# Optimization experiments

Measured on AMD Instinct MI355X. Metric: run time of the kernel, lower is better.

The kernel has to match this reference:

```python
import jax, jax.numpy as jnp
import numpy as np
from jax import lax

H, W = 2048, 2048
KS = 3            # spatial NMS / centroid kernel size
EPS_NMS = 1e-5    # NMS3d eps (threshold=0 branch)
EPS_DIV = 1e-8
BORDER = 1        # int(mrSize=1.0)


def _grid_weights():
    # generate_3dgrid(3, 3, 3) centered: coords = linspace(-k/2+1, k/2, k) = [-0.5, 0.5, 1.5]
    c = np.linspace(-KS / 2 + 1, KS / 2, KS).astype(np.float32)
    g2 = np.stack([np.repeat(c, KS), np.tile(c, KS)], 1)                              # [9,2] (y,x), y-major
    g3 = np.concatenate([np.repeat(c, KS * KS)[:, None], np.tile(g2, (KS, 1))], 1)    # [27,3] (z,y,x)
    # grid.t().view(3,3,3,3): out-channel c holds coordinate c over the 3x3x3 cube (OIHW)
    return jnp.asarray(g3.T.reshape(3, 3, KS, KS))


def _border_mask():
    m = np.ones((H, W), np.float32)
    m[:BORDER] = 0; m[H - BORDER:] = 0; m[:, :BORDER] = 0; m[:, W - BORDER:] = 0
    return jnp.asarray(m)


def setup_inputs() -> dict:
    key = jax.random.key(0)
    k1, k2, k3, k4 = jax.random.split(key, 4)
    return {
        "low": jax.random.uniform(k1, (1, 1, H, W), jnp.float32),
        "cur": jax.random.uniform(k2, (1, 1, H, W), jnp.float32),
        "high": jax.random.uniform(k3, (1, 1, H, W), jnp.float32),
        "aff_resp": jax.random.normal(k4, (1, 4, H, W), jnp.float32),
        "octaveMap": jnp.zeros((1, 1, H, W), jnp.float32),
        "num_features": 4096,
    }


def _core(low, cur, high, aff_resp, octaveMap, num_features):
    resp3d = jnp.concatenate([low, cur, high], axis=1)  # [1,3,H,W] scale cube
    # MaxPool3d(kernel=3, stride=1, padding=(0,1,1)) over (scale,H,W) -> [1,1,H,W]
    mp = lax.reduce_window(resp3d, -jnp.inf, lax.max,
                           (1, 3, 3, 3), (1, 1, 1, 1),
                           [(0, 0), (0, 0), (1, 1), (1, 1)])
    nms = (resp3d - mp + EPS_NMS > 0).astype(resp3d.dtype) * resp3d  # broadcast over 3 scales
    # keep only the center scale, zero 1px border, mask already-taken octave positions
    nmsed = nms[:, 1:2] * _border_mask() * (1.0 - octaveMap)          # [1,1,H,W]
    vals, idxs = lax.top_k(nmsed.reshape(-1), num_features)          # fixed-k selection branch
    # centroid fit: coordinate-weighted 3x3x3 sums / mass via conv2d over the 3 scale channels
    gw = _grid_weights()
    num = lax.conv_general_dilated(resp3d, gw, (1, 1), [(1, 1), (1, 1)])
    den = lax.conv_general_dilated(resp3d, jnp.ones((3, 3, KS, KS), resp3d.dtype),
                                   (1, 1), [(1, 1), (1, 1)])
    sc = num / (den + EPS_DIV)  # [1,3,H,W] = (scale, dy, dx)
    yy, xx = jnp.meshgrid(jnp.arange(H, dtype=sc.dtype), jnp.arange(W, dtype=sc.dtype), indexing="ij")
    sc = jnp.stack([sc[0, 0], sc[0, 1] + yy, sc[0, 2] + xx], 0).reshape(3, -1).T  # [H*W,3]
    sc = sc[idxs] / jnp.array([float(min(H, W)), float(H), float(W)], sc.dtype)   # normalize (s,y,x)
    A = aff_resp.reshape(4, -1).T[idxs].reshape(-1, 2, 2)   # gather per-keypoint affine
    A = sc[:, 0][:, None, None] * A                          # scale * A
    center_xy = jnp.stack([sc[:, 2], sc[:, 1]], axis=1)[:, :, None]  # (x, y) column
    lafs = jnp.concatenate([A, center_xy], axis=2)           # [K,2,3] LAFs
    return vals, lafs, nmsed


def reference(low, cur, high, aff_resp, octaveMap, num_features):
    vals, lafs, nmsed = _core(low, cur, high, aff_resp, octaveMap, num_features)
    octave_new = (octaveMap + nmsed).astype(jnp.uint8)  # updated octave occupancy map
    return vals, lafs, octave_new
```

## Files before the change

### kernel.cpp

```cpp
#include <hip/hip_runtime.h>
#include <cstdint>
#include <cstddef>

#define HH 2048
#define WW 2048
#define NPIX (HH * WW)
#define EPS_NMS 1e-5f
#define EPS_DIV 1e-8f
#define NEG_INF (-3.402823466e+38f)
#define NMS_THREADS 512
#define ROWS 4
#define LCAP 2048
#define SG_CAP 7936
#define NBIN 2048
#define SEL_BLOCKS 64
#define RB_ELEMS 64
#define BUFCAP 4096
#define T0F 0.99854f

typedef unsigned long long u64;


__device__ __forceinline__ float max3(float a, float b, float c) {
    return fmaxf(a, fmaxf(b, c));
}

__device__ __forceinline__ unsigned int aload(const unsigned int* p) {
    return __hip_atomic_load(p, __ATOMIC_RELAXED, __HIP_MEMORY_SCOPE_AGENT);
}

__device__ __forceinline__ void gbar(char* base) {
    __syncthreads();
    if (threadIdx.x == 0) {
        unsigned int* root = (unsigned int*)base;
        unsigned int* gc = (unsigned int*)(base + 64 + ((blockIdx.x & 7) << 6));
        __threadfence();
        if (atomicAdd(gc, 1u) == 7u) atomicAdd(root, 1u);
        while (aload(root) < 8u) __builtin_amdgcn_s_sleep(1);
        __threadfence();
    }
    __syncthreads();
}

__device__ __forceinline__ void pick_bin(const unsigned int* __restrict__ hg,
                                         unsigned int remk_in,
                                         unsigned int* s,
                                         unsigned int* sh_bin,
                                         unsigned int* sh_rem)
{
    const int tid = threadIdx.x;
    unsigned int bins[8], csum = 0;
    #pragma unroll
    for (int i = 0; i < 8; ++i) { bins[i] = aload(&hg[tid * 8 + i]); csum += bins[i]; }
    s[tid] = csum;
    __syncthreads();
    for (int off = 1; off < 256; off <<= 1) {
        unsigned int v = (tid + off < 256) ? s[tid + off] : 0u;
        __syncthreads(); s[tid] += v; __syncthreads();
    }
    unsigned int incl = s[tid], excl = incl - csum, total = s[0];
    if (tid == 0 && total < remk_in) { *sh_bin = 0u; *sh_rem = remk_in; }
    if (incl >= remk_in && excl < remk_in) {
        unsigned int cum = excl; int b = 7;
        for (; b > 0; --b) { cum += bins[b]; if (cum >= remk_in) break; }
        if (cum < remk_in) cum += bins[0];
        *sh_bin = (unsigned int)(tid * 8 + b);
        *sh_rem = remk_in - (cum - bins[b]);
    }
    __syncthreads();
}

__global__ __launch_bounds__(NMS_THREADS) void nms_map_kernel(
    const float* __restrict__ low, const float* __restrict__ cur,
    const float* __restrict__ high, const float* __restrict__ oct,
    float* __restrict__ oct_out, float* __restrict__ vals_out, int n7k,
    u64* __restrict__ cand, unsigned int* __restrict__ cnt,
    unsigned int* __restrict__ hist0, unsigned int cap)
{
    __shared__ unsigned int lcount, lbase, lT;
    __shared__ unsigned int hl[NBIN];
    __shared__ u64 lcand[LCAP];

    const int tid = threadIdx.x;
    const int lane = tid & 63;
    const int x4 = blockIdx.x * 2048 + tid * 4;
    const int y0 = blockIdx.y * ROWS;
    if (tid == 0) { lcount = 0u; lT = 0u; }
    for (int i = tid; i < NBIN; i += NMS_THREADS) hl[i] = 0u;

    if (blockIdx.y < 16) {
        int n4 = n7k >> 2;
        int i = (int)blockIdx.y * NMS_THREADS + tid;
        float4* vz = (float4*)vals_out;
        if (i < n4) vz[i] = make_float4(0.f, 0.f, 0.f, 0.f);
    }
    __syncthreads();

    float4 Lb[2], Cb[2], Hb[2], Ob[2];
    float eLl[2], eLc[2], eLh[2], eRl[2], eRc[2], eRh[2];

    #define ISSUE(t, slot) {                                                      \
        int tt = (t);                                                             \
        if (tt >= 0 && tt < HH) {                                                 \
            int jj = tt * WW + x4;                                                \
            Lb[slot] = *(const float4*)(low  + jj);                               \
            Cb[slot] = *(const float4*)(cur  + jj);                               \
            Hb[slot] = *(const float4*)(high + jj);                               \
            bool doL = (lane == 0)  && (x4 > 0);                                  \
            bool doR = (lane == 63) && (x4 + 4 < WW);                             \
            eLl[slot] = doL ? low[jj - 1]  : NEG_INF;                             \
            eLc[slot] = doL ? cur[jj - 1]  : NEG_INF;                             \
            eLh[slot] = doL ? high[jj - 1] : NEG_INF;                             \
            eRl[slot] = doR ? low[jj + 4]  : NEG_INF;                             \
            eRc[slot] = doR ? cur[jj + 4]  : NEG_INF;                             \
            eRh[slot] = doR ? high[jj + 4] : NEG_INF;                             \
        } else {                                                                  \
            Lb[slot] = Cb[slot] = Hb[slot] =                                      \
                make_float4(NEG_INF, NEG_INF, NEG_INF, NEG_INF);                  \
            eLl[slot] = eLc[slot] = eLh[slot] = NEG_INF;                          \
            eRl[slot] = eRc[slot] = eRh[slot] = NEG_INF;                          \
        }                                                                         \
    }

    #define CONSUME(slot, hzO, cvO) {                                             \
        float4 l = Lb[slot], c = Cb[slot], hh = Hb[slot];                         \
        float4 z;                                                                 \
        z.x = max3(l.x, c.x, hh.x);                                               \
        z.y = max3(l.y, c.y, hh.y);                                               \
        z.z = max3(l.z, c.z, hh.z);                                               \
        z.w = max3(l.w, c.w, hh.w);                                               \
        float zeL = max3(eLl[slot], eLc[slot], eLh[slot]);                        \
        float zeR = max3(eRl[slot], eRc[slot], eRh[slot]);                        \
        float zl = __shfl_up(z.w, 1, 64);                                         \
        float zr = __shfl_down(z.x, 1, 64);                                       \
        if (lane == 0)  zl = zeL;                                                 \
        if (lane == 63) zr = zeR;                                                 \
        hzO.x = max3(zl,  z.x, z.y);                                              \
        hzO.y = max3(z.x, z.y, z.z);                                              \
        hzO.z = max3(z.y, z.z, z.w);                                              \
        hzO.w = max3(z.z, z.w, zr);                                               \
        cvO = c;                                                                  \
    }

    float4 hzA, hzB, hzC, cvB, cvC, cvT;
    ISSUE(y0 - 1, 0)
    ISSUE(y0,     1)
    Ob[0] = *(const float4*)(oct + y0 * WW + x4);
    CONSUME(0, hzA, cvT)
    ISSUE(y0 + 1, 0)
    CONSUME(1, hzB, cvB)

    #pragma unroll
    for (int j = 0; j < ROWS; ++j) {
        int y = y0 + j;
        if (j + 1 < ROWS) {
            ISSUE(y + 2, (j + 1) & 1)
            Ob[(j + 1) & 1] = *(const float4*)(oct + (y + 1) * WW + x4);
        }
        CONSUME(j & 1, hzC, cvC)

        int idx = y * WW + x4;
        float4 o = Ob[j & 1];
        bool yin = (y > 0) && (y < HH - 1);
        float4 ov;
        #define DO_COMP(comp, i)  {                                               \
            float m = max3(hzA.comp, hzB.comp, hzC.comp);                         \
            int xg = x4 + (i);                                                    \
            bool interior = yin && (xg > 0) && (xg < WW - 1);                     \
            float nm = (((cvB.comp - m + EPS_NMS) > 0.0f) && interior)            \
                       ? cvB.comp * (1.0f - o.comp) : 0.0f;                       \
            ov.comp = (float)((unsigned char)(o.comp + nm));                      \
            if (nm > 0.0f) {                                                      \
                unsigned int p = atomicAdd(&lcount, 1u);                          \
                if (p < LCAP)                                                     \
                    lcand[p] = (((u64)__float_as_uint(nm)) << 32)                 \
                               | (unsigned int)(~(idx + (i)));                    \
            }                                                                     \
        }
        DO_COMP(x, 0) DO_COMP(y, 1) DO_COMP(z, 2) DO_COMP(w, 3)
        #undef DO_COMP
        *(float4*)(oct_out + idx) = ov;
        hzA = hzB; hzB = hzC; cvB = cvC;
    }
    #undef ISSUE
    #undef CONSUME

    __syncthreads();
    unsigned int c = lcount < LCAP ? lcount : LCAP;
    if (tid == 0) lbase = atomicAdd(cnt, c);
    __syncthreads();
    unsigned int base = lbase;
    const u64 T0KEY = ((u64)__float_as_uint(T0F)) << 32;
    unsigned int t0c = 0;
    for (unsigned int i = tid; i < c; i += NMS_THREADS) {
        unsigned int p = base + i;
        if (p < cap) {
            u64 k = lcand[i];
            cand[p] = k;
            atomicAdd(&hl[(unsigned int)(k >> 53)], 1u);
            if (k >= T0KEY) ++t0c;
        }
    }
    if (t0c) atomicAdd(&lT, t0c);
    __syncthreads();
    for (int i = tid; i < NBIN; i += NMS_THREADS) {
        unsigned int v = hl[i];
        if (v) atomicAdd(&hist0[i], v);
    }
    if (tid == 0 && lT) atomicAdd(&cnt[2], lT);
}

__global__ __launch_bounds__(256) void select_rank_kernel(
    const u64* __restrict__ cand, u64* __restrict__ SG,
    unsigned int* __restrict__ cnt,
    const unsigned int* __restrict__ hist0, unsigned int* __restrict__ hist1,
    unsigned int cap, int K,
    const float* __restrict__ low, const float* __restrict__ cur,
    const float* __restrict__ high, const float* __restrict__ aff,
    float* __restrict__ out)
{
    __shared__ u64 sgl[SG_CAP];
    __shared__ unsigned int s[256];
    __shared__ unsigned int rnk[RB_ELEMS];
    __shared__ unsigned int sh_bin, sh_rem, lc, lb;
    unsigned int* h = (unsigned int*)sgl;
    u64* buf = sgl + 2048;

    const int tid = threadIdx.x;
    const int bid = blockIdx.x;
    char* barb = (char*)cnt + 128;
    unsigned int n0 = cnt[0];
    unsigned int n = n0; if (n > cap) n = cap;
    const unsigned int stride = SEL_BLOCKS * 256;
    const u64 T0KEY = ((u64)__float_as_uint(T0F)) << 32;

    unsigned int c2 = cnt[2];
    bool use_fast = (n0 <= cap) && (c2 >= (unsigned int)K) && (c2 <= (unsigned int)SG_CAP);
    unsigned int m = 0;

    if (use_fast) {
        if (tid == 0) lc = 0u;
        __syncthreads();
        for (unsigned int i = bid * 256 + tid; i < n; i += stride) {
            u64 key = cand[i];
            if (key >= T0KEY) {
                unsigned int p = atomicAdd(&lc, 1u);
                if (p < BUFCAP) buf[p] = key;
            }
        }
        __syncthreads();
        unsigned int c = lc;
        if (c > BUFCAP) { if (tid == 0) atomicExch(&cnt[4], 1u); c = BUFCAP; }
        if (tid == 0) lb = atomicAdd(&cnt[5], c);
        __syncthreads();
        unsigned int base = lb;
        for (unsigned int i = tid; i < c; i += 256) {
            unsigned int p = base + i;
            if (p < SG_CAP) SG[p] = buf[i];
        }
        gbar(barb);
        if (aload(&cnt[4]) != 0u) use_fast = false;
        else m = aload(&cnt[5]);
    }

    if (!use_fast) {
        pick_bin(hist0, (unsigned int)K, s, &sh_bin, &sh_rem);
        const unsigned int prefix = sh_bin;
        const unsigned int remk   = sh_rem;

        for (int i = tid; i < NBIN; i += 256) h[i] = 0u;
        __syncthreads();
        for (unsigned int i = bid * 256 + tid; i < n; i += stride) {
            unsigned int k32 = (unsigned int)(cand[i] >> 32);
            if ((k32 >> 21) == prefix) atomicAdd(&h[(k32 >> 10) & (NBIN - 1u)], 1u);
        }
        __syncthreads();
        for (int i = tid; i < NBIN; i += 256) { unsigned int v = h[i]; if (v) atomicAdd(&hist1[i], v); }
        gbar(barb + 576);

        pick_bin(hist1, remk, s, &sh_bin, &sh_rem);
        const unsigned int T = (prefix << 11) | sh_bin;

        if (tid == 0) lc = 0u;
        __syncthreads();
        for (unsigned int i = bid * 256 + tid; i < n; i += stride) {
            u64 key = cand[i];
            if ((unsigned int)(key >> 42) >= T) {
                unsigned int p = atomicAdd(&lc, 1u);
                if (p < BUFCAP) buf[p] = key;
            }
        }
        __syncthreads();
        unsigned int c = lc < BUFCAP ? lc : BUFCAP;
        if (tid == 0) lb = atomicAdd(&cnt[1], c);
        __syncthreads();
        unsigned int base = lb;
        for (unsigned int i = tid; i < c; i += 256) {
            unsigned int p = base + i;
            if (p < SG_CAP) SG[p] = buf[i];
        }
        gbar(barb + 2 * 576);
        m = aload(&cnt[1]); if (m > SG_CAP) m = SG_CAP;
    }

    for (unsigned int i = tid; i < m; i += 256) sgl[i] = SG[i];
    __syncthreads();

    const unsigned int wave = (unsigned int)tid >> 6, lane = (unsigned int)tid & 63u;
    for (unsigned int chunk = (unsigned int)bid * RB_ELEMS; chunk < m;
         chunk += (unsigned int)SEL_BLOCKS * RB_ELEMS) {
        u64 my[16];
        unsigned int r[16];
        #pragma unroll
        for (int i = 0; i < 16; ++i) {
            unsigned int e = chunk + wave * 16 + i;
            my[i] = (e < m) ? sgl[e] : ~0ull;
            r[i] = 0u;
        }
        for (unsigned int j = lane; j < m; j += 64) {
            u64 key = sgl[j];
            #pragma unroll
            for (int i = 0; i < 16; ++i) r[i] += (unsigned int)(key > my[i]);
        }
        #pragma unroll
        for (int i = 0; i < 16; ++i) {
            #pragma unroll
            for (int off = 32; off > 0; off >>= 1)
                r[i] += __shfl_down(r[i], off, 64);
            if (lane == 0) rnk[wave * 16 + i] = r[i];
        }
        __syncthreads();

        if (tid < RB_ELEMS) {
            unsigned int e = chunk + (unsigned int)tid;
            if (e < m) {
                unsigned int rank = rnk[tid];
                if (rank < (unsigned int)K) {
                    u64 my_key = sgl[e];
                    float val = __uint_as_float((unsigned int)(my_key >> 32));
                    unsigned int idx = ~((unsigned int)my_key);
                    out[rank] = val;
                    float* laf = out + K + (size_t)rank * 6;
                    int y = (int)(idx >> 11), x = (int)(idx & (WW - 1));
                    const float ccw[3] = {-0.5f, 0.5f, 1.5f};
                    float den = 0.0f, nz = 0.0f, ny = 0.0f, nx = 0.0f;
                    #pragma unroll
                    for (int dy = -1; dy <= 1; ++dy) {
                        int yy = y + dy;
                        if (yy < 0 || yy >= HH) continue;
                        #pragma unroll
                        for (int dx = -1; dx <= 1; ++dx) {
                            int xx = x + dx;
                            if (xx < 0 || xx >= WW) continue;
                            int jj = yy * WW + xx;
                            float v0 = low[jj], v1 = cur[jj], v2 = high[jj];
                            float ssum = v0 + v1 + v2;
                            den += ssum;
                            nz += -0.5f * v0 + 0.5f * v1 + 1.5f * v2;
                            ny += ccw[dy + 1] * ssum;
                            nx += ccw[dx + 1] * ssum;
                        }
                    }
                    float inv = 1.0f / (den + EPS_DIV);
                    float s_n = (nz * inv) * (1.0f / 2048.0f);
                    float y_n = (ny * inv + (float)y) * (1.0f / 2048.0f);
                    float x_n = (nx * inv + (float)x) * (1.0f / 2048.0f);
                    float a0 = aff[idx], a1 = aff[NPIX + idx];
                    float a2 = aff[2 * NPIX + idx], a3 = aff[3 * NPIX + idx];
                    laf[0] = s_n * a0; laf[1] = s_n * a1; laf[2] = x_n;
                    laf[3] = s_n * a2; laf[4] = s_n * a3; laf[5] = y_n;
                }
            }
        }
        __syncthreads();
    }
}

extern "C" void kernel_launch(void* const* d_in, const int* in_sizes, int n_in,
                              void* d_out, int out_size, void* d_ws, size_t ws_size,
                              hipStream_t stream) {
    const float* low  = (const float*)d_in[0];
    const float* cur  = (const float*)d_in[1];
    const float* high = (const float*)d_in[2];
    const float* aff  = (const float*)d_in[3];
    const float* oct  = (const float*)d_in[4];
    int K = (out_size - NPIX) / 7;
    float* out = (float*)d_out;

    char* ws = (char*)d_ws;
    unsigned int* cnt   = (unsigned int*)ws;
    unsigned int* hist0 = (unsigned int*)(ws + 4096);
    unsigned int* hist1 = (unsigned int*)(ws + 12288);
    u64* SG             = (u64*)(ws + 20480);
    const size_t cand_off = 98304;
    u64* cand           = (u64*)(ws + cand_off);
    size_t cap_sz = ws_size > cand_off ? (ws_size - cand_off) / 8 : 0;
    if (cap_sz > (size_t)NPIX) cap_sz = (size_t)NPIX;
    unsigned int cap = (unsigned int)cap_sz;

    hipMemsetAsync(ws, 0, 20480, stream);

    dim3 gb(WW / 2048, HH / ROWS, 1);
    nms_map_kernel<<<gb, NMS_THREADS, 0, stream>>>(low, cur, high, oct,
                                                   out + (size_t)7 * K,
                                                   out, 7 * K, cand, cnt, hist0, cap);
    select_rank_kernel<<<SEL_BLOCKS, 256, 0, stream>>>(cand, SG, cnt, hist0, hist1,
                                                       cap, K, low, cur, high, aff, out);
}
```

Before: 219.3 us.

## Fuse NMS map and top-k selection into one kernel with last-block crew

Merges the NMS/candidate kernel and the select-rank kernel into one launch. The last 64 blocks to finish the map phase, identified by a ticket counter, become a crew that runs the selection and ranking behind grid barriers. The per-block global histogram build is moved off the hot path into the slow fallback only. Output zeroing now covers only the unfilled ranks, done at the end. The change removes one kernel launch and the histogram atomics, but the crew must spin-wait until all blocks finish, and it relies on all 512 blocks being co-resident or draining in order.

```diff
diff --git a/kernel.cpp b/kernel.cpp
--- a/kernel.cpp
+++ b/kernel.cpp
@@ -8,14 +8,15 @@
 #define EPS_NMS 1e-5f
 #define EPS_DIV 1e-8f
 #define NEG_INF (-3.402823466e+38f)
-#define NMS_THREADS 512
-#define ROWS 4
+#define ROWS 8
 #define LCAP 2048
-#define SG_CAP 7936
+#define SG_CAP 7680
 #define NBIN 2048
-#define SEL_BLOCKS 64
+#define NMS_BLOCKS 512
+#define CREW 64
+#define TICKET_MIN (NMS_BLOCKS - CREW)
 #define RB_ELEMS 64
-#define BUFCAP 4096
+#define BUFCAP 1024
 #define T0F 0.99854f
 
 typedef unsigned long long u64;
@@ -29,11 +30,11 @@
     return __hip_atomic_load(p, __ATOMIC_RELAXED, __HIP_MEMORY_SCOPE_AGENT);
 }
 
-__device__ __forceinline__ void gbar(char* base) {
+__device__ __forceinline__ void gbar(char* base, unsigned int crewid) {
     __syncthreads();
     if (threadIdx.x == 0) {
         unsigned int* root = (unsigned int*)base;
-        unsigned int* gc = (unsigned int*)(base + 64 + ((blockIdx.x & 7) << 6));
+        unsigned int* gc = (unsigned int*)(base + 64 + ((crewid & 7u) << 6));
         __threadfence();
         if (atomicAdd(gc, 1u) == 7u) atomicAdd(root, 1u);
         while (aload(root) < 8u) __builtin_amdgcn_s_sleep(1);
@@ -70,30 +71,28 @@
     __syncthreads();
 }
 
-__global__ __launch_bounds__(NMS_THREADS) void nms_map_kernel(
+__global__ __launch_bounds__(256) void fused_kernel(
     const float* __restrict__ low, const float* __restrict__ cur,
     const float* __restrict__ high, const float* __restrict__ oct,
-    float* __restrict__ oct_out, float* __restrict__ vals_out, int n7k,
+    const float* __restrict__ aff,
+    float* __restrict__ oct_out, float* __restrict__ out, int K,
     u64* __restrict__ cand, unsigned int* __restrict__ cnt,
-    unsigned int* __restrict__ hist0, unsigned int cap)
+    unsigned int* __restrict__ hist0, unsigned int* __restrict__ hist1,
+    u64* __restrict__ SG, unsigned int cap)
 {
-    __shared__ unsigned int lcount, lbase, lT;
-    __shared__ unsigned int hl[NBIN];
-    __shared__ u64 lcand[LCAP];
+    __shared__ u64 sgl[SG_CAP];
+    __shared__ unsigned int s[256];
+    __shared__ unsigned int rnk[RB_ELEMS];
+    __shared__ unsigned int lcount, lbase, lT, lticket, lc, lb, sh_bin, sh_rem;
+    u64* lcand = sgl;
+    u64* buf = sgl + 2048;
+    unsigned int* h = (unsigned int*)sgl;
 
     const int tid = threadIdx.x;
     const int lane = tid & 63;
-    const int x4 = blockIdx.x * 2048 + tid * 4;
+    const int x4 = blockIdx.x * 1024 + tid * 4;
     const int y0 = blockIdx.y * ROWS;
     if (tid == 0) { lcount = 0u; lT = 0u; }
-    for (int i = tid; i < NBIN; i += NMS_THREADS) hl[i] = 0u;
-
-    if (blockIdx.y < 16) {
-        int n4 = n7k >> 2;
-        int i = (int)blockIdx.y * NMS_THREADS + tid;
-        float4* vz = (float4*)vals_out;
-        if (i < n4) vz[i] = make_float4(0.f, 0.f, 0.f, 0.f);
-    }
     __syncthreads();
 
     float4 Lb[2], Cb[2], Hb[2], Ob[2];
@@ -187,61 +186,50 @@
 
     __syncthreads();
     unsigned int c = lcount < LCAP ? lcount : LCAP;
-    if (tid == 0) lbase = atomicAdd(cnt, c);
+    if (tid == 0) lbase = atomicAdd(&cnt[0], c);
     __syncthreads();
     unsigned int base = lbase;
     const u64 T0KEY = ((u64)__float_as_uint(T0F)) << 32;
     unsigned int t0c = 0;
-    for (unsigned int i = tid; i < c; i += NMS_THREADS) {
+    for (unsigned int i = tid; i < c; i += 256) {
         unsigned int p = base + i;
         if (p < cap) {
             u64 k = lcand[i];
             cand[p] = k;
-            atomicAdd(&hl[(unsigned int)(k >> 53)], 1u);
             if (k >= T0KEY) ++t0c;
         }
     }
     if (t0c) atomicAdd(&lT, t0c);
     __syncthreads();
-    for (int i = tid; i < NBIN; i += NMS_THREADS) {
-        unsigned int v = hl[i];
-        if (v) atomicAdd(&hist0[i], v);
-    }
     if (tid == 0 && lT) atomicAdd(&cnt[2], lT);
-}
-
-__global__ __launch_bounds__(256) void select_rank_kernel(
-    const u64* __restrict__ cand, u64* __restrict__ SG,
-    unsigned int* __restrict__ cnt,
-    const unsigned int* __restrict__ hist0, unsigned int* __restrict__ hist1,
-    unsigned int cap, int K,
-    const float* __restrict__ low, const float* __restrict__ cur,
-    const float* __restrict__ high, const float* __restrict__ aff,
-    float* __restrict__ out)
-{
-    __shared__ u64 sgl[SG_CAP];
-    __shared__ unsigned int s[256];
-    __shared__ unsigned int rnk[RB_ELEMS];
-    __shared__ unsigned int sh_bin, sh_rem, lc, lb;
-    unsigned int* h = (unsigned int*)sgl;
-    u64* buf = sgl + 2048;
-
-    const int tid = threadIdx.x;
-    const int bid = blockIdx.x;
+
+    __syncthreads();
+    if (tid == 0) {
+        __threadfence();
+        lticket = atomicAdd(&cnt[8], 1u);
+    }
+    __syncthreads();
+    unsigned int ticket = lticket;
+    if (ticket < (unsigned int)TICKET_MIN) return;
+    unsigned int crewid = ticket - (unsigned int)TICKET_MIN;
+    if (tid == 0) {
+        while (aload(&cnt[8]) < (unsigned int)NMS_BLOCKS) __builtin_amdgcn_s_sleep(2);
+        __threadfence();
+    }
+    __syncthreads();
+
     char* barb = (char*)cnt + 128;
-    unsigned int n0 = cnt[0];
+    unsigned int n0 = aload(&cnt[0]);
     unsigned int n = n0; if (n > cap) n = cap;
-    const unsigned int stride = SEL_BLOCKS * 256;
-    const u64 T0KEY = ((u64)__float_as_uint(T0F)) << 32;
-
-    unsigned int c2 = cnt[2];
+    unsigned int c2 = aload(&cnt[2]);
+    const unsigned int stride = CREW * 256;
     bool use_fast = (n0 <= cap) && (c2 >= (unsigned int)K) && (c2 <= (unsigned int)SG_CAP);
     unsigned int m = 0;
 
     if (use_fast) {
         if (tid == 0) lc = 0u;
         __syncthreads();
-        for (unsigned int i = bid * 256 + tid; i < n; i += stride) {
+        for (unsigned int i = crewid * 256 + tid; i < n; i += stride) {
             u64 key = cand[i];
             if (key >= T0KEY) {
                 unsigned int p = atomicAdd(&lc, 1u);
@@ -249,41 +237,49 @@
             }
         }
         __syncthreads();
-        unsigned int c = lc;
-        if (c > BUFCAP) { if (tid == 0) atomicExch(&cnt[4], 1u); c = BUFCAP; }
-        if (tid == 0) lb = atomicAdd(&cnt[5], c);
-        __syncthreads();
-        unsigned int base = lb;
-        for (unsigned int i = tid; i < c; i += 256) {
-            unsigned int p = base + i;
+        unsigned int cc = lc;
+        if (cc > BUFCAP) { if (tid == 0) atomicExch(&cnt[4], 1u); cc = BUFCAP; }
+        if (tid == 0) lb = atomicAdd(&cnt[5], cc);
+        __syncthreads();
+        unsigned int b2 = lb;
+        for (unsigned int i = tid; i < cc; i += 256) {
+            unsigned int p = b2 + i;
             if (p < SG_CAP) SG[p] = buf[i];
         }
-        gbar(barb);
+        gbar(barb, crewid);
         if (aload(&cnt[4]) != 0u) use_fast = false;
         else m = aload(&cnt[5]);
+    } else {
+        gbar(barb, crewid);
     }
 
     if (!use_fast) {
+        for (int i = tid; i < NBIN; i += 256) h[i] = 0u;
+        __syncthreads();
+        for (unsigned int i = crewid * 256 + tid; i < n; i += stride)
+            atomicAdd(&h[(unsigned int)(cand[i] >> 53)], 1u);
+        __syncthreads();
+        for (int i = tid; i < NBIN; i += 256) { unsigned int v = h[i]; if (v) atomicAdd(&hist0[i], v); }
+        gbar(barb + 576, crewid);
         pick_bin(hist0, (unsigned int)K, s, &sh_bin, &sh_rem);
         const unsigned int prefix = sh_bin;
         const unsigned int remk   = sh_rem;
 
         for (int i = tid; i < NBIN; i += 256) h[i] = 0u;
         __syncthreads();
-        for (unsigned int i = bid * 256 + tid; i < n; i += stride) {
+        for (unsigned int i = crewid * 256 + tid; i < n; i += stride) {
             unsigned int k32 = (unsigned int)(cand[i] >> 32);
             if ((k32 >> 21) == prefix) atomicAdd(&h[(k32 >> 10) & (NBIN - 1u)], 1u);
         }
         __syncthreads();
         for (int i = tid; i < NBIN; i += 256) { unsigned int v = h[i]; if (v) atomicAdd(&hist1[i], v); }
-        gbar(barb + 576);
-
+        gbar(barb + 2 * 576, crewid);
         pick_bin(hist1, remk, s, &sh_bin, &sh_rem);
         const unsigned int T = (prefix << 11) | sh_bin;
 
         if (tid == 0) lc = 0u;
         __syncthreads();
-        for (unsigned int i = bid * 256 + tid; i < n; i += stride) {
+        for (unsigned int i = crewid * 256 + tid; i < n; i += stride) {
             u64 key = cand[i];
             if ((unsigned int)(key >> 42) >= T) {
                 unsigned int p = atomicAdd(&lc, 1u);
@@ -291,24 +287,24 @@
             }
         }
         __syncthreads();
-        unsigned int c = lc < BUFCAP ? lc : BUFCAP;
-        if (tid == 0) lb = atomicAdd(&cnt[1], c);
-        __syncthreads();
-        unsigned int base = lb;
-        for (unsigned int i = tid; i < c; i += 256) {
-            unsigned int p = base + i;
+        unsigned int cc = lc < BUFCAP ? lc : BUFCAP;
+        if (tid == 0) lb = atomicAdd(&cnt[1], cc);
+        __syncthreads();
+        unsigned int b2 = lb;
+        for (unsigned int i = tid; i < cc; i += 256) {
+            unsigned int p = b2 + i;
             if (p < SG_CAP) SG[p] = buf[i];
         }
-        gbar(barb + 2 * 576);
+        gbar(barb + 3 * 576, crewid);
         m = aload(&cnt[1]); if (m > SG_CAP) m = SG_CAP;
     }
 
     for (unsigned int i = tid; i < m; i += 256) sgl[i] = SG[i];
     __syncthreads();
 
-    const unsigned int wave = (unsigned int)tid >> 6, lane = (unsigned int)tid & 63u;
-    for (unsigned int chunk = (unsigned int)bid * RB_ELEMS; chunk < m;
-         chunk += (unsigned int)SEL_BLOCKS * RB_ELEMS) {
+    const unsigned int wave = (unsigned int)tid >> 6, ln = (unsigned int)tid & 63u;
+    for (unsigned int chunk = crewid * RB_ELEMS; chunk < m;
+         chunk += (unsigned int)CREW * RB_ELEMS) {
         u64 my[16];
         unsigned int r[16];
         #pragma unroll
@@ -317,7 +313,7 @@
             my[i] = (e < m) ? sgl[e] : ~0ull;
             r[i] = 0u;
         }
-        for (unsigned int j = lane; j < m; j += 64) {
+        for (unsigned int j = ln; j < m; j += 64) {
             u64 key = sgl[j];
             #pragma unroll
             for (int i = 0; i < 16; ++i) r[i] += (unsigned int)(key > my[i]);
@@ -327,7 +323,7 @@
             #pragma unroll
             for (int off = 32; off > 0; off >>= 1)
                 r[i] += __shfl_down(r[i], off, 64);
-            if (lane == 0) rnk[wave * 16 + i] = r[i];
+            if (ln == 0) rnk[wave * 16 + i] = r[i];
         }
         __syncthreads();
 
@@ -374,6 +370,13 @@
         }
         __syncthreads();
     }
+
+    unsigned int mm = m < (unsigned int)K ? m : (unsigned int)K;
+    for (unsigned int r2 = mm + crewid * 256 + tid; r2 < (unsigned int)K; r2 += stride) {
+        out[r2] = 0.0f;
+        float* laf = out + K + (size_t)r2 * 6;
+        laf[0] = 0.f; laf[1] = 0.f; laf[2] = 0.f; laf[3] = 0.f; laf[4] = 0.f; laf[5] = 0.f;
+    }
 }
 
 extern "C" void kernel_launch(void* const* d_in, const int* in_sizes, int n_in,
@@ -400,10 +403,8 @@
 
     hipMemsetAsync(ws, 0, 20480, stream);
 
-    dim3 gb(WW / 2048, HH / ROWS, 1);
-    nms_map_kernel<<<gb, NMS_THREADS, 0, stream>>>(low, cur, high, oct,
-                                                   out + (size_t)7 * K,
-                                                   out, 7 * K, cand, cnt, hist0, cap);
-    select_rank_kernel<<<SEL_BLOCKS, 256, 0, stream>>>(cand, SG, cnt, hist0, hist1,
-                                                       cap, K, low, cur, high, aff, out);
-}
+    dim3 gb(WW / 1024, HH / ROWS, 1);
+    fused_kernel<<<gb, 256, 0, stream>>>(low, cur, high, oct, aff,
+                                         out + (size_t)7 * K, out, K,
+                                         cand, cnt, hist0, hist1, SG, cap);
+}
```

Result: slower. 232.4 us (+6.0%).
